# Kernel optimization log

Hardware: AMD Instinct MI355X
Metric: run time of the kernel (lower is better)

The kernel has to match this reference:

```python
import jax, jax.numpy as jnp
import numpy as np

B, T, D = 8, 1024, 1024
F, NB, FPB, ES, NE = 64, 4, 16, 4, 16
DFE, DRH, DEH = 128, 256, 512
RIN = D + DFE  # router input dim (hidden + feature embedding)
TEMP = 1.0
BUNDLE_TOPK = 2
EXPERT_TOPK = 2
LN_EPS = 1e-5


def setup_inputs() -> dict:
    key = jax.random.key(0)
    ks = jax.random.split(key, 24)
    s = 0.02
    n = lambda k, shp, sc=s: jax.random.normal(k, shp, dtype=jnp.float32) * sc
    return {
        "hidden": jax.random.normal(ks[0], (B, T, D), dtype=jnp.float32),
        "feat": jax.random.uniform(ks[1], (B, T, F), dtype=jnp.float32),
        "ln_g": jnp.ones((D,), jnp.float32),
        "ln_b": jnp.zeros((D,), jnp.float32),
        "stage_W": n(ks[2], (F, DFE)),
        "stage_b": jnp.zeros((DFE,), jnp.float32),
        "bproj_W": n(ks[3], (NB, FPB, DFE)),
        "bproj_b": jnp.zeros((NB, DFE), jnp.float32),
        "br_W1": n(ks[4], (RIN, DRH)),
        "br_b1": jnp.zeros((DRH,), jnp.float32),
        "br_W2": n(ks[5], (DRH, NB)),
        "br_b2": jnp.zeros((NB,), jnp.float32),
        "ir_W1": n(ks[6], (NB, RIN, DRH)),
        "ir_b1": jnp.zeros((NB, DRH), jnp.float32),
        "ir_W2": n(ks[7], (NB, DRH, ES)),
        "ir_b2": jnp.zeros((NB, ES), jnp.float32),
        "ex_W1": n(ks[8], (NE, D, DEH)),
        "ex_b1": jnp.zeros((NE, DEH), jnp.float32),
        "ex_W2": n(ks[9], (NE, DEH, D)),
        "ex_b2": jnp.zeros((NE, D), jnp.float32),
        "alpha": jnp.float32(1.0),
    }


def _topk_softmax(logits, temp, k):
    # scale by temperature, keep top-k logits, softmax (renormalized over kept)
    s = logits / temp
    if k is not None and k < s.shape[-1]:
        thr = jax.lax.top_k(s, k)[0][..., -1:]
        s = jnp.where(s >= thr, s, -jnp.inf)
    return jax.nn.softmax(s, axis=-1)


def _gelu(x):
    return jax.nn.gelu(x, approximate=False)  # torch nn.GELU default = exact erf


def reference(hidden, feat, ln_g, ln_b, stage_W, stage_b, bproj_W, bproj_b,
              br_W1, br_b1, br_W2, br_b2, ir_W1, ir_b1, ir_W2, ir_b2,
              ex_W1, ex_b1, ex_W2, ex_b2, alpha):
    # pre-LN
    mu = hidden.mean(-1, keepdims=True)
    var = ((hidden - mu) ** 2).mean(-1, keepdims=True)
    h_norm = (hidden - mu) * jax.lax.rsqrt(var + LN_EPS) * ln_g + ln_b  # [B,T,D]

    # stage feature embedding (stage_feat_idx = all 64 features here)
    sfe = feat @ stage_W + stage_b  # [B,T,DFE]
    bundle_in = jnp.concatenate([h_norm, sfe], axis=-1)  # [B,T,RIN]
    bundle_logits = _gelu(bundle_in @ br_W1 + br_b1) @ br_W2 + br_b2  # [B,T,NB]
    bundle_weights = _topk_softmax(bundle_logits, TEMP, BUNDLE_TOPK)

    # intra-bundle routers (vectorized over the 4 bundles)
    # bundle_feat_idx_g = [g*16 .. g*16+15] -> contiguous reshape is exact gather
    bfeat = feat.reshape(B, T, NB, FPB)
    bemb = jnp.einsum('btgf,gfe->btge', bfeat, bproj_W) + bproj_b  # [B,T,NB,DFE]
    iin = jnp.concatenate(
        [jnp.broadcast_to(h_norm[:, :, None, :], (B, T, NB, D)), bemb], axis=-1)
    ih = _gelu(jnp.einsum('btgi,gih->btgh', iin, ir_W1) + ir_b1)
    intra_logits = jnp.einsum('btgh,ghe->btge', ih, ir_W2) + ir_b2  # [B,T,NB,ES]
    intra_weights = _topk_softmax(intra_logits, TEMP, EXPERT_TOPK)

    gate_weights = (bundle_weights[..., None] * intra_weights).reshape(B, T, NE)
    gate_logits = (bundle_logits[..., None] + intra_logits).reshape(B, T, NE)

    # all experts run densely on h_norm, combined by gate weights
    eh = _gelu(jnp.einsum('btd,edh->bteh', h_norm, ex_W1) + ex_b1)  # [B,T,NE,DEH]
    eo = jnp.einsum('bteh,ehd->bted', eh, ex_W2) + ex_b2            # [B,T,NE,D]
    stage_delta = jnp.einsum('bte,bted->btd', gate_weights, eo)

    next_hidden = hidden + alpha * stage_delta  # alpha_scale = 1.0, eval dropout
    return (next_hidden, gate_weights, gate_logits, bundle_weights,
            bundle_logits, stage_delta)
```

## Files before the change

### kernel.cpp

```cpp
#include <hip/hip_runtime.h>


typedef unsigned short u16;
typedef u16 u16x8 __attribute__((ext_vector_type(8)));
typedef __bf16 bf16x8 __attribute__((ext_vector_type(8)));
typedef float f32x4 __attribute__((ext_vector_type(4)));

#define M_TOK 8192

__device__ __forceinline__ float bf2f(u16 u) {
  return __uint_as_float(((unsigned)u) << 16);
}
__device__ __forceinline__ u16 f2bf(float f) {
  unsigned u = __float_as_uint(f);
  unsigned r = (u + 0x7fffu + ((u >> 16) & 1u)) >> 16;
  return (u16)r;
}
__device__ __forceinline__ void split3(float x, u16& p0, u16& p1, u16& p2) {
  p0 = f2bf(x);
  float r = x - bf2f(p0);
  p1 = f2bf(r);
  float r2 = r - bf2f(p1);
  p2 = f2bf(r2);
}
__device__ __forceinline__ float gelu_exact(float x) {
  return 0.5f * x * (1.f + erff(x * 0.70710678118654752f));
}
__device__ __forceinline__ void gload16(const u16* g, u16* l) {
  __builtin_amdgcn_global_load_lds(
      (const __attribute__((address_space(1))) void*)g,
      (__attribute__((address_space(3))) void*)l, 16, 0, 0);
}

__global__ void probe_k(int* flag) {
  int lane = threadIdx.x & 63;
  int lq = lane & 15, quad = lane >> 4;
  u16x8 au, bu;
#pragma unroll
  for (int j = 0; j < 8; ++j) {
    int k = quad * 8 + j;
    float av = (k == 0) ? (float)lq : (k == 1 ? 1.f : 0.f);
    float bv = (k == 0) ? 1.f : (k == 1 ? 2.f * (float)lq : 0.f);
    au[j] = f2bf(av);
    bu[j] = f2bf(bv);
  }
  f32x4 acc = {};
  acc = __builtin_amdgcn_mfma_f32_16x16x32_bf16(
      __builtin_bit_cast(bf16x8, au), __builtin_bit_cast(bf16x8, bu), acc, 0, 0, 0);
  bool okg = true, oks = true;
#pragma unroll
  for (int rr = 0; rr < 4; ++rr) {
    float vg = (float)((quad * 4 + rr) + 2 * lq);
    float vs = (float)(lq + 2 * (quad * 4 + rr));
    okg = okg && (acc[rr] == vg);
    oks = oks && (acc[rr] == vs);
  }
  unsigned long long bg = __ballot(okg), bs = __ballot(oks);
  if (threadIdx.x == 0) *flag = (bg == ~0ull) ? 0 : ((bs == ~0ull) ? 1 : 0);
}

__global__ __launch_bounds__(256) void transpose_k(const float* __restrict__ src,
                                                   u16* __restrict__ dst,
                                                   int R, int C) {
  src += (size_t)blockIdx.z * R * C;
  dst += (size_t)blockIdx.z * R * C;
  __shared__ u16 tile[32][33];
  int r0 = blockIdx.x * 32, c0 = blockIdx.y * 32;
  int tx = threadIdx.x, ty = threadIdx.y;
#pragma unroll
  for (int k = 0; k < 4; ++k) {
    int r = r0 + ty + k * 8;
    if (r < R && c0 + tx < C) tile[ty + k * 8][tx] = f2bf(src[(size_t)r * C + c0 + tx]);
  }
  __syncthreads();
#pragma unroll
  for (int k = 0; k < 4; ++k) {
    int c = c0 + ty + k * 8;
    if (c < C && r0 + tx < R) dst[(size_t)c * R + r0 + tx] = tile[tx][ty + k * 8];
  }
}

__global__ __launch_bounds__(256) void transpose_k3(const float* __restrict__ src,
                                                    u16* __restrict__ dst,
                                                    int R, int C, size_t PS) {
  src += (size_t)blockIdx.z * R * C;
  dst += (size_t)blockIdx.z * R * C;
  __shared__ float tile[32][33];
  int r0 = blockIdx.x * 32, c0 = blockIdx.y * 32;
  int tx = threadIdx.x, ty = threadIdx.y;
#pragma unroll
  for (int k = 0; k < 4; ++k) {
    int r = r0 + ty + k * 8;
    if (r < R && c0 + tx < C) tile[ty + k * 8][tx] = src[(size_t)r * C + c0 + tx];
  }
  __syncthreads();
#pragma unroll
  for (int k = 0; k < 4; ++k) {
    int c = c0 + ty + k * 8;
    if (c < C && r0 + tx < R) {
      u16 p0, p1, p2;
      split3(tile[tx][ty + k * 8], p0, p1, p2);
      size_t idx = (size_t)c * R + r0 + tx;
      dst[idx] = p0;
      dst[PS + idx] = p1;
      dst[2 * PS + idx] = p2;
    }
  }
}

__global__ __launch_bounds__(256) void ln_k(const float* __restrict__ h,
                                            const float* __restrict__ gam,
                                            const float* __restrict__ bet,
                                            u16* __restrict__ out) {
  const size_t PS = (size_t)M_TOK * 1024;
  int wave = threadIdx.x >> 6, lane = threadIdx.x & 63;
  int t = blockIdx.x * 4 + wave;
  const float4* row4 = (const float4*)(h + (size_t)t * 1024);
  float x[16];
#pragma unroll
  for (int k = 0; k < 4; ++k) {
    float4 v = row4[lane * 4 + k];
    x[k * 4 + 0] = v.x; x[k * 4 + 1] = v.y; x[k * 4 + 2] = v.z; x[k * 4 + 3] = v.w;
  }
  float s = 0.f, ss = 0.f;
#pragma unroll
  for (int i = 0; i < 16; ++i) { s += x[i]; ss += x[i] * x[i]; }
#pragma unroll
  for (int m = 1; m < 64; m <<= 1) { s += __shfl_xor(s, m); ss += __shfl_xor(ss, m); }
  float mu = s * (1.f / 1024.f);
  float var = ss * (1.f / 1024.f) - mu * mu;
  float inv = rsqrtf(var + 1e-5f);
  const float4* g4 = (const float4*)gam;
  const float4* b4 = (const float4*)bet;
  u16x8 o0[3], o1[3];
#pragma unroll
  for (int k = 0; k < 4; ++k) {
    float4 g = g4[lane * 4 + k];
    float4 b = b4[lane * 4 + k];
    float vals[4] = {(x[k * 4 + 0] - mu) * inv * g.x + b.x,
                     (x[k * 4 + 1] - mu) * inv * g.y + b.y,
                     (x[k * 4 + 2] - mu) * inv * g.z + b.z,
                     (x[k * 4 + 3] - mu) * inv * g.w + b.w};
#pragma unroll
    for (int e = 0; e < 4; ++e) {
      u16 p0, p1, p2;
      split3(vals[e], p0, p1, p2);
      int sl = k * 4 + e;
      if (sl < 8) { o0[0][sl] = p0; o0[1][sl] = p1; o0[2][sl] = p2; }
      else { o1[0][sl - 8] = p0; o1[1][sl - 8] = p1; o1[2][sl - 8] = p2; }
    }
  }
  size_t base = (size_t)t * 1024 + lane * 16;
#pragma unroll
  for (int p = 0; p < 3; ++p) {
    *(u16x8*)(out + p * PS + base) = o0[p];
    *(u16x8*)(out + p * PS + base + 8) = o1[p];
  }
}

__global__ __launch_bounds__(128) void feat_k(const float* __restrict__ feat,
    const float* __restrict__ stW, const float* __restrict__ stb,
    const float* __restrict__ bpW, const float* __restrict__ bpb,
    u16* __restrict__ sfe3, u16* __restrict__ bemb3) {
  const size_t S_PS = (size_t)M_TOK * 128;
  const size_t E_PS = (size_t)4 * M_TOK * 128;
  int t = blockIdx.x;
  int n = threadIdx.x;
  __shared__ float fsh[64];
  if (n < 64) fsh[n] = feat[(size_t)t * 64 + n];
  __syncthreads();
  float s = stb[n];
  for (int k = 0; k < 64; ++k) s += fsh[k] * stW[k * 128 + n];
  {
    u16 p0, p1, p2;
    split3(s, p0, p1, p2);
    size_t idx = (size_t)t * 128 + n;
    sfe3[idx] = p0; sfe3[S_PS + idx] = p1; sfe3[2 * S_PS + idx] = p2;
  }
#pragma unroll
  for (int g = 0; g < 4; ++g) {
    float v = bpb[g * 128 + n];
#pragma unroll
    for (int j = 0; j < 16; ++j)
      v += fsh[g * 16 + j] * bpW[(g * 16 + j) * 128 + n];
    u16 p0, p1, p2;
    split3(v, p0, p1, p2);
    size_t idx = ((size_t)g * M_TOK + t) * 128 + n;
    bemb3[idx] = p0; bemb3[E_PS + idx] = p1; bemb3[2 * E_PS + idx] = p2;
  }
}

__global__ __launch_bounds__(256) void rgemm_k(
    const u16* __restrict__ hn3, const u16* __restrict__ sfe3,
    const u16* __restrict__ bemb3, const u16* __restrict__ Bt3,
    const float* __restrict__ bias0, const float* __restrict__ bias1,
    float* __restrict__ ih, const int* __restrict__ flagp) {
  __shared__ __align__(16) u16 shA[3][64 * 64];
  __shared__ __align__(16) u16 shB[3][64 * 64];
  const int tid = threadIdx.x;
  const int wave = tid >> 6, lane = tid & 63;
  const int gz = blockIdx.x >> 2;
  const int bn64 = (blockIdx.x & 3) * 64;
  const int bm64 = blockIdx.y * 64;
  const size_t A_PS = (size_t)M_TOK * 1024;
  const size_t S_PS = (size_t)M_TOK * 128;
  const size_t E_PS = (size_t)4 * M_TOK * 128;
  const size_t B_PS = (size_t)5 * 256 * 1152;
  const u16* AexB = (gz == 0) ? sfe3 : (bemb3 + (size_t)(gz - 1) * M_TOK * 128);
  const size_t Aex_PS = (gz == 0) ? S_PS : E_PS;
  const u16* BtP = Bt3 + (size_t)gz * 256 * 1152;

  f32x4 acc[2][2] = {};
  const int lq = lane & 15, quad = lane >> 4;
  const int wm = (wave >> 1) * 32, wn = (wave & 1) * 32;

  for (int kit = 0; kit < 18; ++kit) {
    int k0 = kit * 64;
#pragma unroll
    for (int half = 0; half < 2; ++half) {
      int ch = half * 256 + tid;
      int r = ch >> 3, ssl = ch & 7;
      int c = ssl ^ (r & 7);
      int gk = k0 + c * 8;
#pragma unroll
      for (int p = 0; p < 3; ++p) {
        const u16* gA = (gk < 1024)
            ? (hn3 + (size_t)p * A_PS + (size_t)(bm64 + r) * 1024 + gk)
            : (AexB + (size_t)p * Aex_PS + (size_t)(bm64 + r) * 128 + (gk - 1024));
        const u16* gB = BtP + (size_t)p * B_PS + (size_t)(bn64 + r) * 1152 + gk;
        gload16(gA, &shA[p][(half * 256 + wave * 64) * 8]);
        gload16(gB, &shB[p][(half * 256 + wave * 64) * 8]);
      }
    }
    __syncthreads();
#pragma unroll
    for (int ks = 0; ks < 2; ++ks) {
      bf16x8 af[3][2], bfr[3][2];
#pragma unroll
      for (int i = 0; i < 2; ++i) {
        int r = wm + i * 16 + lq;
        int cc = (ks * 4 + quad) ^ (r & 7);
        int rb = wn + i * 16 + lq;
        int cb = (ks * 4 + quad) ^ (rb & 7);
#pragma unroll
        for (int p = 0; p < 3; ++p) {
          af[p][i] = *(const bf16x8*)&shA[p][(r * 8 + cc) * 8];
          bfr[p][i] = *(const bf16x8*)&shB[p][(rb * 8 + cb) * 8];
        }
      }
#pragma unroll
      for (int i = 0; i < 2; ++i)
#pragma unroll
        for (int j = 0; j < 2; ++j) {
          acc[i][j] = __builtin_amdgcn_mfma_f32_16x16x32_bf16(af[0][i], bfr[0][j], acc[i][j], 0, 0, 0);
          acc[i][j] = __builtin_amdgcn_mfma_f32_16x16x32_bf16(af[0][i], bfr[1][j], acc[i][j], 0, 0, 0);
          acc[i][j] = __builtin_amdgcn_mfma_f32_16x16x32_bf16(af[1][i], bfr[0][j], acc[i][j], 0, 0, 0);
          acc[i][j] = __builtin_amdgcn_mfma_f32_16x16x32_bf16(af[0][i], bfr[2][j], acc[i][j], 0, 0, 0);
          acc[i][j] = __builtin_amdgcn_mfma_f32_16x16x32_bf16(af[1][i], bfr[1][j], acc[i][j], 0, 0, 0);
          acc[i][j] = __builtin_amdgcn_mfma_f32_16x16x32_bf16(af[2][i], bfr[0][j], acc[i][j], 0, 0, 0);
        }
    }
    __syncthreads();
  }

  const int fl = *flagp;
  const float* biasP = (gz == 0) ? bias0 : (bias1 + (gz - 1) * 256);
#pragma unroll
  for (int i = 0; i < 2; ++i) {
#pragma unroll
    for (int j = 0; j < 2; ++j) {
#pragma unroll
      for (int rr = 0; rr < 4; ++rr) {
        int m, col;
        if (fl == 0) {
          m = bm64 + wm + i * 16 + quad * 4 + rr;
          col = bn64 + wn + j * 16 + lq;
        } else {
          m = bm64 + wm + i * 16 + lq;
          col = bn64 + wn + j * 16 + quad * 4 + rr;
        }
        ih[((size_t)gz * M_TOK + m) * 256 + col] = gelu_exact(acc[i][j][rr] + biasP[col]);
      }
    }
  }
}

template <int MODE>
__global__ __launch_bounds__(256) void gemm128_k(
    const u16* __restrict__ A0, const u16* __restrict__ Bt0,
    const float* __restrict__ bias0, const float* __restrict__ gwf,
    float* __restrict__ out32, u16* __restrict__ out16,
    int e0, int first, const int* __restrict__ flagp) {
  __shared__ __align__(16) u16 shA[128 * 64];
  __shared__ __align__(16) u16 shB[128 * 64];
  const int tid = threadIdx.x;
  const int wave = tid >> 6, lane = tid & 63;
  int bm, bn, ez = 0;
  if constexpr (MODE == 1) {
    ez = blockIdx.x & 7;
    bn = (blockIdx.x >> 3) * 128;
  } else {
    bn = blockIdx.x * 128;
  }
  bm = blockIdx.y * 128;

  const u16* BtP;
  int KITER;
  if constexpr (MODE == 1) {
    BtP = Bt0 + (size_t)ez * 512 * 1024;
    KITER = 16;
  } else {
    BtP = Bt0;
    KITER = 64;
  }

  f32x4 acc[4][4] = {};
  const int lq = lane & 15, quad = lane >> 4;
  const int wr = (wave >> 1) * 64, wc = (wave & 1) * 64;

  for (int kit = 0; kit < KITER; ++kit) {
    int k0 = kit * 64;
#pragma unroll
    for (int q = 0; q < 4; ++q) {
      int ch = q * 256 + tid;
      int r = ch >> 3, ssl = ch & 7;
      int c = ssl ^ (r & 7);
      int gk = k0 + c * 8;
      const u16 *gA, *gB;
      if constexpr (MODE == 1) {
        gA = A0 + (size_t)(bm + r) * 1024 + gk;
        gB = BtP + (size_t)(bn + r) * 1024 + gk;
      } else {
        int el = gk >> 9, kk = gk & 511;
        gA = A0 + ((size_t)el * M_TOK + bm + r) * 512 + kk;
        gB = BtP + ((size_t)el * 1024 + bn + r) * 512 + kk;
      }
      gload16(gA, &shA[(q * 256 + wave * 64) * 8]);
      gload16(gB, &shB[(q * 256 + wave * 64) * 8]);
    }
    __syncthreads();
#pragma unroll
    for (int ks = 0; ks < 2; ++ks) {
      bf16x8 af[4], bfr[4];
#pragma unroll
      for (int i = 0; i < 4; ++i) {
        int r = wr + i * 16 + lq;
        int cc = (ks * 4 + quad) ^ (r & 7);
        af[i] = *(const bf16x8*)&shA[(r * 8 + cc) * 8];
        int rb = wc + i * 16 + lq;
        int cb = (ks * 4 + quad) ^ (rb & 7);
        bfr[i] = *(const bf16x8*)&shB[(rb * 8 + cb) * 8];
      }
#pragma unroll
      for (int i = 0; i < 4; ++i)
#pragma unroll
        for (int j = 0; j < 4; ++j)
          acc[i][j] = __builtin_amdgcn_mfma_f32_16x16x32_bf16(af[i], bfr[j], acc[i][j], 0, 0, 0);
    }
    __syncthreads();
  }

  const int fl = *flagp;
  const float* biasP = nullptr;
  if constexpr (MODE == 1) biasP = bias0 + (e0 + ez) * 512;

#pragma unroll
  for (int i = 0; i < 4; ++i) {
#pragma unroll
    for (int j = 0; j < 4; ++j) {
#pragma unroll
      for (int rr = 0; rr < 4; ++rr) {
        int m, col;
        if (fl == 0) {
          m = bm + wr + i * 16 + quad * 4 + rr;
          col = bn + wc + j * 16 + lq;
        } else {
          m = bm + wr + i * 16 + lq;
          col = bn + wc + j * 16 + quad * 4 + rr;
        }
        float v = acc[i][j][rr];
        if constexpr (MODE == 1) {
          float w = gwf[(size_t)m * 16 + e0 + ez];
          out16[((size_t)ez * M_TOK + m) * 512 + col] =
              f2bf(w * gelu_exact(v + biasP[col]));
        } else {
          size_t idx = (size_t)m * 1024 + col;
          float prev = first ? 0.f : out32[idx];
          out32[idx] = prev + v;
        }
      }
    }
  }
}

__device__ __forceinline__ void topk2_softmax4(const float* s, float* w) {
  float m1 = fmaxf(fmaxf(s[0], s[1]), fmaxf(s[2], s[3]));
  float m2 = -1e30f;
  bool seen = false;
#pragma unroll
  for (int i = 0; i < 4; ++i) {
    if (s[i] == m1 && !seen) seen = true;
    else m2 = fmaxf(m2, s[i]);
  }
  float e[4];
  float sum = 0.f;
#pragma unroll
  for (int i = 0; i < 4; ++i) {
    e[i] = (s[i] >= m2) ? expf(s[i] - m1) : 0.f;
    sum += e[i];
  }
  float invs = 1.f / sum;
#pragma unroll
  for (int i = 0; i < 4; ++i) w[i] = e[i] * invs;
}

__global__ __launch_bounds__(256) void gating_k(
    const float* __restrict__ ih_all, const float* __restrict__ brW2,
    const float* __restrict__ brb2, const float* __restrict__ irW2,
    const float* __restrict__ irb2, float* __restrict__ gwf,
    float* __restrict__ o_gw, float* __restrict__ o_gl,
    float* __restrict__ o_bw, float* __restrict__ o_bl) {
  int wave = threadIdx.x >> 6, lane = threadIdx.x & 63;
  int t = blockIdx.x * 4 + wave;
  const float4* bw4 = (const float4*)brW2;
  const float4* iw4 = (const float4*)irW2;
  float v[20];
#pragma unroll
  for (int i = 0; i < 20; ++i) v[i] = 0.f;
  const float* bh = ih_all + (size_t)t * 256;
#pragma unroll
  for (int jj = 0; jj < 4; ++jj) {
    int k = jj * 64 + lane;
    float h = bh[k];
    float4 wv = bw4[k];
    v[0] += h * wv.x; v[1] += h * wv.y; v[2] += h * wv.z; v[3] += h * wv.w;
  }
#pragma unroll
  for (int g = 0; g < 4; ++g) {
    const float* ihg = ih_all + ((size_t)(1 + g) * M_TOK + t) * 256;
#pragma unroll
    for (int jj = 0; jj < 4; ++jj) {
      int k = jj * 64 + lane;
      float h = ihg[k];
      float4 wv = iw4[g * 256 + k];
      v[4 + g * 4 + 0] += h * wv.x; v[4 + g * 4 + 1] += h * wv.y;
      v[4 + g * 4 + 2] += h * wv.z; v[4 + g * 4 + 3] += h * wv.w;
    }
  }
#pragma unroll
  for (int i = 0; i < 20; ++i)
#pragma unroll
    for (int m = 1; m < 64; m <<= 1) v[i] += __shfl_xor(v[i], m);
  if (lane == 0) {
    float blog[4], ilog[4][4];
#pragma unroll
    for (int c = 0; c < 4; ++c) blog[c] = v[c] + brb2[c];
#pragma unroll
    for (int g = 0; g < 4; ++g)
#pragma unroll
      for (int e = 0; e < 4; ++e) ilog[g][e] = v[4 + g * 4 + e] + irb2[g * 4 + e];
    float bw[4];
    topk2_softmax4(blog, bw);
#pragma unroll
    for (int g = 0; g < 4; ++g) {
      float iw[4];
      topk2_softmax4(ilog[g], iw);
#pragma unroll
      for (int e = 0; e < 4; ++e) {
        int idx = g * 4 + e;
        float wv = bw[g] * iw[e];
        gwf[(size_t)t * 16 + idx] = wv;
        o_gw[(size_t)t * 16 + idx] = wv;
        o_gl[(size_t)t * 16 + idx] = blog[g] + ilog[g][e];
      }
      o_bw[(size_t)t * 4 + g] = bw[g];
      o_bl[(size_t)t * 4 + g] = blog[g];
    }
  }
}

__global__ __launch_bounds__(256) void combine_k(
    const float* __restrict__ gwf, const float* __restrict__ b2,
    const float* __restrict__ hidden, const float* __restrict__ alpha_p,
    float* __restrict__ o_next, float* __restrict__ o_delta) {
  int row = blockIdx.x;
  float a = alpha_p[0];
  float wb[16];
#pragma unroll
  for (int e = 0; e < 16; ++e) wb[e] = gwf[(size_t)row * 16 + e];
#pragma unroll
  for (int k = 0; k < 4; ++k) {
    int c = threadIdx.x + k * 256;
    float s = 0.f;
#pragma unroll
    for (int e = 0; e < 16; ++e) s += wb[e] * b2[e * 1024 + c];
    size_t idx = (size_t)row * 1024 + c;
    float d = o_delta[idx] + s;
    o_delta[idx] = d;
    o_next[idx] = hidden[idx] + a * d;
  }
}

extern "C" void kernel_launch(void* const* d_in, const int* in_sizes, int n_in,
                              void* d_out, int out_size, void* d_ws, size_t ws_size,
                              hipStream_t stream) {
  (void)in_sizes; (void)n_in; (void)out_size; (void)ws_size;
  const float* hidden  = (const float*)d_in[0];
  const float* feat    = (const float*)d_in[1];
  const float* ln_g    = (const float*)d_in[2];
  const float* ln_b    = (const float*)d_in[3];
  const float* stage_W = (const float*)d_in[4];
  const float* stage_b = (const float*)d_in[5];
  const float* bproj_W = (const float*)d_in[6];
  const float* bproj_b = (const float*)d_in[7];
  const float* br_W1   = (const float*)d_in[8];
  const float* br_b1   = (const float*)d_in[9];
  const float* br_W2   = (const float*)d_in[10];
  const float* br_b2   = (const float*)d_in[11];
  const float* ir_W1   = (const float*)d_in[12];
  const float* ir_b1   = (const float*)d_in[13];
  const float* ir_W2   = (const float*)d_in[14];
  const float* ir_b2   = (const float*)d_in[15];
  const float* ex_W1   = (const float*)d_in[16];
  const float* ex_b1   = (const float*)d_in[17];
  const float* ex_W2   = (const float*)d_in[18];
  const float* ex_b2   = (const float*)d_in[19];
  const float* alpha   = (const float*)d_in[20];

  char* w = (char*)d_ws;
  size_t off = 0;
  auto alloc = [&](size_t bytes) {
    void* p = w + off;
    off += (bytes + 255) & ~(size_t)255;
    return p;
  };
  int* flagp   = (int*)alloc(256);
  u16* wt3     = (u16*)alloc(3ull * 5 * 256 * 1152 * 2);
  u16* hn3     = (u16*)alloc(3ull * M_TOK * 1024 * 2);
  float* gwf   = (float*)alloc((size_t)M_TOK * 16 * 4);
  char* region = (char*)alloc(88090000);
  u16* sfe3   = (u16*)region;
  u16* bemb3  = (u16*)(region + 6291456);
  float* ih   = (float*)(region + 6291456 + 25165824);
  u16* w1t_g  = (u16*)region;
  u16* w2t_g  = (u16*)(region + 8388608);
  u16* Gbuf   = (u16*)(region + 16777216);

  float* out = (float*)d_out;
  float* o_next  = out;
  float* o_gw    = out + 8388608;
  float* o_gl    = o_gw + 131072;
  float* o_bw    = o_gl + 131072;
  float* o_bl    = o_bw + 32768;
  float* o_delta = o_bl + 32768;

  probe_k<<<1, 64, 0, stream>>>(flagp);

  transpose_k3<<<dim3(36, 8, 1), dim3(32, 8), 0, stream>>>(
      br_W1, wt3, 1152, 256, (size_t)5 * 256 * 1152);
  transpose_k3<<<dim3(36, 8, 4), dim3(32, 8), 0, stream>>>(
      ir_W1, wt3 + 256 * 1152, 1152, 256, (size_t)5 * 256 * 1152);

  ln_k<<<2048, 256, 0, stream>>>(hidden, ln_g, ln_b, hn3);
  feat_k<<<8192, 128, 0, stream>>>(feat, stage_W, stage_b, bproj_W, bproj_b, sfe3, bemb3);

  rgemm_k<<<dim3(20, 128), 256, 0, stream>>>(hn3, sfe3, bemb3, wt3, br_b1, ir_b1, ih, flagp);
  gating_k<<<2048, 256, 0, stream>>>(ih, br_W2, br_b2, ir_W2, ir_b2, gwf,
                                     o_gw, o_gl, o_bw, o_bl);

  for (int grp = 0; grp < 2; ++grp) {
    transpose_k<<<dim3(32, 16, 8), dim3(32, 8), 0, stream>>>(
        ex_W1 + (size_t)grp * 8 * 1024 * 512, w1t_g, 1024, 512);
    transpose_k<<<dim3(16, 32, 8), dim3(32, 8), 0, stream>>>(
        ex_W2 + (size_t)grp * 8 * 512 * 1024, w2t_g, 512, 1024);
    gemm128_k<1><<<dim3(32, 64), 256, 0, stream>>>(hn3, w1t_g, ex_b1, gwf,
                                                   nullptr, Gbuf, grp * 8, 0, flagp);
    gemm128_k<2><<<dim3(8, 64), 256, 0, stream>>>(Gbuf, w2t_g, nullptr, nullptr,
                                                  o_delta, nullptr, grp * 8,
                                                  grp == 0 ? 1 : 0, flagp);
  }

  combine_k<<<8192, 256, 0, stream>>>(gwf, ex_b2, hidden, alpha, o_next, o_delta);
}
```

Measured before the change: 867.2 us.

## Replace expert FFN1 GEMM with 256x256-tile, 8-wave pipelined kernel

Adds a new ffn1_k kernel for the first expert GEMM. It uses 256x256 output tiles with 512 threads and double-buffered, XOR-swizzled LDS filled by direct global-to-LDS loads. Loads for the next k-steps are interleaved between four MFMA phases, using fine-grained barriers, vmcnt waits and s_setprio to overlap memory with compute. The aim is more data reuse per tile and better latency hiding than the old 128x128 gemm128_k<1>. In exchange it needs more registers and LDS per block (two blocks per CU) and adds extra barrier synchronisation.

Result: no change. 850.4 us (-1.9%).

```diff
diff --git a/kernel.cpp b/kernel.cpp
--- a/kernel.cpp
+++ b/kernel.cpp
@@ -31,6 +31,15 @@
       (const __attribute__((address_space(1))) void*)g,
       (__attribute__((address_space(3))) void*)l, 16, 0, 0);
 }
+
+#define BAR()                               \
+  do {                                      \
+    asm volatile("" ::: "memory");          \
+    __builtin_amdgcn_s_barrier();           \
+    asm volatile("" ::: "memory");          \
+  } while (0)
+#define WAITV6() asm volatile("s_waitcnt vmcnt(6)" ::: "memory")
+#define WAITV0() asm volatile("s_waitcnt vmcnt(0)" ::: "memory")
 
 __global__ void probe_k(int* flag) {
   int lane = threadIdx.x & 63;
@@ -280,6 +289,153 @@
           col = bn64 + wn + j * 16 + quad * 4 + rr;
         }
         ih[((size_t)gz * M_TOK + m) * 256 + col] = gelu_exact(acc[i][j][rr] + biasP[col]);
+      }
+    }
+  }
+}
+
+__global__ __launch_bounds__(512, 2) void ffn1_k(
+    const u16* __restrict__ A0, const u16* __restrict__ Bt0,
+    const float* __restrict__ b1all, const float* __restrict__ gwf,
+    u16* __restrict__ out16, int e0, const int* __restrict__ flagp) {
+  __shared__ __align__(16) u16 ldsA[2][2][128 * 64];
+  __shared__ __align__(16) u16 ldsB[2][2][128 * 64];
+  const int tid = threadIdx.x;
+  const int wid = tid >> 6, lane = tid & 63;
+  const int lq = lane & 15, quad = lane >> 4;
+  const int swz = lq & 7;
+  const int wmb = (wid >> 2) * 64;
+  const int wnb = (wid & 3) * 32;
+  const int ez = blockIdx.x >> 1;
+  const int bn = (blockIdx.x & 1) * 256;
+  const int bm = blockIdx.y * 256;
+  const u16* BtP = Bt0 + (size_t)ez * 512 * 1024;
+
+  f32x4 acc[8][4] = {};
+  bf16x8 af[4][2], bfr[4][2];
+
+  auto stageA = [&](int tt, int h) {
+#pragma unroll
+    for (int q = 0; q < 2; ++q) {
+      int ch = q * 512 + tid;
+      int r = ch >> 3, ssl = ch & 7;
+      int c = ssl ^ (r & 7);
+      gload16(A0 + (size_t)(bm + h * 128 + r) * 1024 + tt * 64 + c * 8,
+              &ldsA[tt & 1][h][(q * 512 + (tid & ~63)) * 8]);
+    }
+  };
+  auto stageB = [&](int tt, int h) {
+#pragma unroll
+    for (int q = 0; q < 2; ++q) {
+      int ch = q * 512 + tid;
+      int r = ch >> 3, ssl = ch & 7;
+      int c = ssl ^ (r & 7);
+      gload16(BtP + (size_t)(bn + h * 128 + r) * 1024 + tt * 64 + c * 8,
+              &ldsB[tt & 1][h][(q * 512 + (tid & ~63)) * 8]);
+    }
+  };
+
+  stageA(0, 0); stageB(0, 0); stageB(0, 1); stageA(0, 1);
+  stageA(1, 0); stageB(1, 0); stageB(1, 1);
+  WAITV6();
+  BAR();
+
+#pragma unroll 2
+  for (int t = 0; t < 16; ++t) {
+    const int buf = t & 1;
+#pragma unroll
+    for (int i = 0; i < 4; ++i) {
+      int rh = wmb + i * 16 + lq;
+#pragma unroll
+      for (int ks = 0; ks < 2; ++ks)
+        af[i][ks] = *(const bf16x8*)&ldsA[buf][0][(rh * 8 + ((ks * 4 + quad) ^ swz)) * 8];
+    }
+#pragma unroll
+    for (int g = 0; g < 4; ++g) {
+      int rh = wnb + (g & 1) * 16 + lq;
+#pragma unroll
+      for (int ks = 0; ks < 2; ++ks)
+        bfr[g][ks] = *(const bf16x8*)&ldsB[buf][g >> 1][(rh * 8 + ((ks * 4 + quad) ^ swz)) * 8];
+    }
+    if (t + 1 < 16) stageA(t + 1, 1);
+    BAR();
+    __builtin_amdgcn_s_setprio(1);
+#pragma unroll
+    for (int i = 0; i < 4; ++i)
+#pragma unroll
+      for (int g = 0; g < 2; ++g) {
+        acc[i][g] = __builtin_amdgcn_mfma_f32_16x16x32_bf16(af[i][0], bfr[g][0], acc[i][g], 0, 0, 0);
+        acc[i][g] = __builtin_amdgcn_mfma_f32_16x16x32_bf16(af[i][1], bfr[g][1], acc[i][g], 0, 0, 0);
+      }
+    __builtin_amdgcn_s_setprio(0);
+    BAR();
+    if (t + 2 < 16) stageA(t + 2, 0);
+    BAR();
+    __builtin_amdgcn_s_setprio(1);
+#pragma unroll
+    for (int i = 0; i < 4; ++i)
+#pragma unroll
+      for (int g = 2; g < 4; ++g) {
+        acc[i][g] = __builtin_amdgcn_mfma_f32_16x16x32_bf16(af[i][0], bfr[g][0], acc[i][g], 0, 0, 0);
+        acc[i][g] = __builtin_amdgcn_mfma_f32_16x16x32_bf16(af[i][1], bfr[g][1], acc[i][g], 0, 0, 0);
+      }
+    __builtin_amdgcn_s_setprio(0);
+    BAR();
+#pragma unroll
+    for (int i = 0; i < 4; ++i) {
+      int rh = wmb + i * 16 + lq;
+#pragma unroll
+      for (int ks = 0; ks < 2; ++ks)
+        af[i][ks] = *(const bf16x8*)&ldsA[buf][1][(rh * 8 + ((ks * 4 + quad) ^ swz)) * 8];
+    }
+    if (t + 2 < 16) stageB(t + 2, 0);
+    BAR();
+    __builtin_amdgcn_s_setprio(1);
+#pragma unroll
+    for (int i = 0; i < 4; ++i)
+#pragma unroll
+      for (int g = 0; g < 2; ++g) {
+        acc[4 + i][g] = __builtin_amdgcn_mfma_f32_16x16x32_bf16(af[i][0], bfr[g][0], acc[4 + i][g], 0, 0, 0);
+        acc[4 + i][g] = __builtin_amdgcn_mfma_f32_16x16x32_bf16(af[i][1], bfr[g][1], acc[4 + i][g], 0, 0, 0);
+      }
+    __builtin_amdgcn_s_setprio(0);
+    BAR();
+    if (t + 2 < 16) stageB(t + 2, 1);
+    BAR();
+    __builtin_amdgcn_s_setprio(1);
+#pragma unroll
+    for (int i = 0; i < 4; ++i)
+#pragma unroll
+      for (int g = 2; g < 4; ++g) {
+        acc[4 + i][g] = __builtin_amdgcn_mfma_f32_16x16x32_bf16(af[i][0], bfr[g][0], acc[4 + i][g], 0, 0, 0);
+        acc[4 + i][g] = __builtin_amdgcn_mfma_f32_16x16x32_bf16(af[i][1], bfr[g][1], acc[4 + i][g], 0, 0, 0);
+      }
+    __builtin_amdgcn_s_setprio(0);
+    if (t == 14) { WAITV0(); } else { WAITV6(); }
+    BAR();
+  }
+
+  const int fl = *flagp;
+  const float* biasP = b1all + (e0 + ez) * 512;
+#pragma unroll
+  for (int f = 0; f < 8; ++f) {
+    int mbase = bm + wmb + (f & 3) * 16 + (f >> 2) * 128;
+#pragma unroll
+    for (int g = 0; g < 4; ++g) {
+      int cbase = bn + wnb + (g & 1) * 16 + (g >> 1) * 128;
+#pragma unroll
+      for (int rr = 0; rr < 4; ++rr) {
+        int m, col;
+        if (fl == 0) {
+          m = mbase + quad * 4 + rr;
+          col = cbase + lq;
+        } else {
+          m = mbase + lq;
+          col = cbase + quad * 4 + rr;
+        }
+        float w = gwf[(size_t)m * 16 + e0 + ez];
+        out16[((size_t)ez * M_TOK + m) * 512 + col] =
+            f2bf(w * gelu_exact(acc[f][g][rr] + biasP[col]));
       }
     }
   }
@@ -573,8 +729,8 @@
         ex_W1 + (size_t)grp * 8 * 1024 * 512, w1t_g, 1024, 512);
     transpose_k<<<dim3(16, 32, 8), dim3(32, 8), 0, stream>>>(
         ex_W2 + (size_t)grp * 8 * 512 * 1024, w2t_g, 512, 1024);
-    gemm128_k<1><<<dim3(32, 64), 256, 0, stream>>>(hn3, w1t_g, ex_b1, gwf,
-                                                   nullptr, Gbuf, grp * 8, 0, flagp);
+    ffn1_k<<<dim3(16, 32), 512, 0, stream>>>(hn3, w1t_g, ex_b1, gwf,
+                                             Gbuf, grp * 8, flagp);
     gemm128_k<2><<<dim3(8, 64), 256, 0, stream>>>(Gbuf, w2t_g, nullptr, nullptr,
                                                   o_delta, nullptr, grp * 8,
                                                   grp == 0 ? 1 : 0, flagp);
```
